# Performance work log

Measured on AMD Instinct MI355X. Metric: run time of the kernel, lower is better.

The kernel has to match this reference:

```python
import jax, jax.numpy as jnp
import numpy as np

B, C, W, H = 4, 256, 64, 64
CQK = C // 8  # 32


def setup_inputs() -> dict:
    key = jax.random.key(0)
    ks = jax.random.split(key, 8)
    scale = 0.02
    x = jax.random.normal(ks[0], (B, C, W, H), dtype=jnp.float32)
    wq = jax.random.normal(ks[1], (CQK, C), dtype=jnp.float32) * scale
    bq = jnp.zeros((CQK,), dtype=jnp.float32)
    wk = jax.random.normal(ks[2], (CQK, C), dtype=jnp.float32) * scale
    bk = jnp.zeros((CQK,), dtype=jnp.float32)
    wv = jax.random.normal(ks[3], (C, C), dtype=jnp.float32) * scale
    bv = jnp.zeros((C,), dtype=jnp.float32)
    gamma = jnp.zeros((1,), dtype=jnp.float32)
    return {"x": x, "wq": wq, "bq": bq, "wk": wk, "bk": bk,
            "wv": wv, "bv": bv, "gamma": gamma}


def reference(x, wq, bq, wk, bk, wv, bv, gamma):
    b, c, w, h = x.shape
    n = w * h
    xf = x.reshape(b, c, n)                         # b, C, N
    # 1x1 convs == channel matmuls
    q = jnp.einsum('oc,bcn->bno', wq, xf) + bq      # b, N, Cqk
    k = jnp.einsum('oc,bcn->bon', wk, xf) + bk[:, None]  # b, Cqk, N
    v = jnp.einsum('oc,bcn->bon', wv, xf) + bv[:, None]  # b, C, N
    energy = jnp.einsum('bic,bcj->bij', q, k)       # b, N, N
    attention = jax.nn.softmax(energy, axis=-1)     # b, N, N
    # out[b,c,i] = sum_j v[b,c,j] * attention[b,i,j]
    out = jnp.einsum('bcj,bij->bci', v, attention)  # b, C, N
    out = out.reshape(b, c, w, h)
    out = gamma[0] * out + x
    return out, attention
```

## Files before the change

### kernel.cpp

```cpp
#include <hip/hip_runtime.h>

#define NB 4
#define NC 256
#define NN 4096
#define NQK 32

typedef short short8 __attribute__((ext_vector_type(8)));
typedef float f32x4 __attribute__((ext_vector_type(4)));

#define MFMA16(a, b, c) __builtin_amdgcn_mfma_f32_16x16x32_bf16((a), (b), (c), 0, 0, 0)

__device__ __forceinline__ unsigned short f2bf(float f) {
  unsigned int u = __builtin_bit_cast(unsigned int, f);
  u += 0x7fffu + ((u >> 16) & 1u);
  return (unsigned short)(u >> 16);
}

__global__ void k_prep(const float* __restrict__ wq, const float* __restrict__ wk,
                       const float* __restrict__ wv,
                       unsigned short* __restrict__ wqb, unsigned short* __restrict__ wkb,
                       unsigned short* __restrict__ wvb) {
  int i = blockIdx.x * 256 + threadIdx.x;
  if (i < NQK * NC) { wqb[i] = f2bf(wq[i]); wkb[i] = f2bf(wk[i]); }
  wvb[i] = f2bf(wv[i]);
}

__global__ void k_tr(const float* __restrict__ x, unsigned short* __restrict__ xT) {
  __shared__ unsigned short lds[64][66];
  int b = blockIdx.z, c0 = blockIdx.y * 64, n0 = blockIdx.x * 64;
  int t = threadIdx.x;
  int nl = t & 63, cq = t >> 6;
  const float* xp = x + ((size_t)(b * NC + c0)) * NN + n0;
#pragma unroll
  for (int r = 0; r < 16; ++r) {
    int cl = r * 4 + cq;
    lds[cl][nl] = f2bf(xp[(size_t)cl * NN + nl]);
  }
  __syncthreads();
  unsigned short* xo = xT + ((size_t)(b * NN + n0)) * NC + c0;
#pragma unroll
  for (int r = 0; r < 16; ++r) {
    int n2 = r * 4 + cq;
    xo[(size_t)n2 * NC + nl] = lds[nl][n2];
  }
}

__global__ __launch_bounds__(256) void k_proj(
    const unsigned short* __restrict__ xT,
    const unsigned short* __restrict__ wqb, const unsigned short* __restrict__ wkb,
    const unsigned short* __restrict__ wvb,
    const float* __restrict__ bq, const float* __restrict__ bk,
    const float* __restrict__ bv,
    unsigned short* __restrict__ qb, unsigned short* __restrict__ kTb,
    unsigned short* __restrict__ vb) {
  __shared__ unsigned short ldsv[256][68];
  int b = blockIdx.y, n0 = blockIdx.x * 64;
  int t = threadIdx.x, w = t >> 6, l = t & 63, lm = l & 15, lk = l >> 4;
  f32x4 qa[2] = {}, ka[2] = {}, va[16] = {};
  const unsigned short* xrow = xT + ((size_t)(b * NN + n0 + w * 16 + lm)) * NC + lk * 8;
#pragma unroll
  for (int kk = 0; kk < 8; ++kk) {
    short8 a = *(const short8*)(xrow + kk * 32);
    const unsigned short* wqp = wqb + lm * NC + kk * 32 + lk * 8;
    const unsigned short* wkp = wkb + lm * NC + kk * 32 + lk * 8;
    qa[0] = MFMA16(a, *(const short8*)(wqp), qa[0]);
    qa[1] = MFMA16(a, *(const short8*)(wqp + 16 * NC), qa[1]);
    ka[0] = MFMA16(a, *(const short8*)(wkp), ka[0]);
    ka[1] = MFMA16(a, *(const short8*)(wkp + 16 * NC), ka[1]);
#pragma unroll
    for (int ct = 0; ct < 16; ++ct) {
      const unsigned short* wvp = wvb + (ct * 16 + lm) * NC + kk * 32 + lk * 8;
      va[ct] = MFMA16(a, *(const short8*)(wvp), va[ct]);
    }
  }
  int nrow = n0 + w * 16 + lk * 4;
#pragma unroll
  for (int f = 0; f < 2; ++f) {
    float bqv = bq[f * 16 + lm], bkv = bk[f * 16 + lm];
#pragma unroll
    for (int r = 0; r < 4; ++r) {
      size_t o = ((size_t)(b * NN + nrow + r)) * NQK + f * 16 + lm;
      qb[o] = f2bf(qa[f][r] + bqv);
      kTb[o] = f2bf(ka[f][r] + bkv);
    }
  }
#pragma unroll
  for (int ct = 0; ct < 16; ++ct) {
    float bvv = bv[ct * 16 + lm];
#pragma unroll
    for (int r = 0; r < 4; ++r)
      ldsv[ct * 16 + lm][w * 16 + lk * 4 + r] = f2bf(va[ct][r] + bvv);
  }
  __syncthreads();
#pragma unroll
  for (int rep = 0; rep < 64; ++rep) {
    int c = rep * 4 + (t >> 6);
    int n = t & 63;
    vb[((size_t)(b * NC + c)) * NN + n0 + n] = ldsv[c][n];
  }
}

__global__ __launch_bounds__(512) void k_attn(
    const unsigned short* __restrict__ qb, const unsigned short* __restrict__ kTb,
    const unsigned short* __restrict__ vb, const float* __restrict__ x,
    const float* __restrict__ gamma, float* __restrict__ out,
    float* __restrict__ attn) {
  __shared__ unsigned short ldsv[256][72];
  __shared__ unsigned short ldsp[64][72];
  __shared__ float ldsd[64][2];
  int b = blockIdx.y, i0 = blockIdx.x * 64;
  int t = threadIdx.x, w = t >> 6, l = t & 63, lm = l & 15, lk = l >> 4;
  int is = w & 3, jh = w >> 2;
  int cg = w & 3, ih = w >> 2;
  const f32x4 z = {0.f, 0.f, 0.f, 0.f};

  short8 qa = *(const short8*)(qb + ((size_t)(b * NN + i0 + is * 16 + lm)) * NQK + lk * 8);
  const unsigned short* kbase = kTb + (size_t)b * NN * NQK + lk * 8;

  float ds0[4] = {0.f, 0.f, 0.f, 0.f};
  for (int j0 = jh * 2048; j0 < jh * 2048 + 2048; j0 += 32) {
    short8 kf0 = *(const short8*)(kbase + (size_t)(j0 + lm) * NQK);
    short8 kf1 = *(const short8*)(kbase + (size_t)(j0 + 16 + lm) * NQK);
    f32x4 e0 = MFMA16(qa, kf0, z);
    f32x4 e1 = MFMA16(qa, kf1, z);
#pragma unroll
    for (int r = 0; r < 4; ++r) ds0[r] += __expf(e0[r]) + __expf(e1[r]);
  }
#pragma unroll
  for (int m = 1; m < 16; m <<= 1)
#pragma unroll
    for (int r = 0; r < 4; ++r) ds0[r] += __shfl_xor(ds0[r], m);
  if (lm == 0) {
#pragma unroll
    for (int r = 0; r < 4; ++r) ldsd[is * 16 + lk * 4 + r][jh] = ds0[r];
  }
  __syncthreads();
  float dinv[4];
#pragma unroll
  for (int r = 0; r < 4; ++r) {
    int row = is * 16 + lk * 4 + r;
    dinv[r] = 1.0f / (ldsd[row][0] + ldsd[row][1]);
  }

  f32x4 acc[4][2] = {};
  float g = gamma[0];
  float* attn_b = attn + (size_t)b * NN * NN;
  for (int j0 = 0; j0 < NN; j0 += 64) {
    __syncthreads();
#pragma unroll
    for (int it = 0; it < 4; ++it) {
      int qid = it * 512 + t;
      int row = qid >> 3, part = qid & 7;
      *(short8*)(&ldsv[row][part * 8]) =
          *(const short8*)(vb + ((size_t)(b * NC + row)) * NN + j0 + part * 8);
    }
    int jb = j0 + jh * 32;
    short8 kf0 = *(const short8*)(kbase + (size_t)(jb + lm) * NQK);
    short8 kf1 = *(const short8*)(kbase + (size_t)(jb + 16 + lm) * NQK);
    f32x4 e0 = MFMA16(qa, kf0, z);
    f32x4 e1 = MFMA16(qa, kf1, z);
    int irow = i0 + is * 16 + lk * 4;
#pragma unroll
    for (int r = 0; r < 4; ++r) {
      float p0 = __expf(e0[r]) * dinv[r];
      float p1 = __expf(e1[r]) * dinv[r];
      __builtin_nontemporal_store(p0, &attn_b[(size_t)(irow + r) * NN + jb + lm]);
      __builtin_nontemporal_store(p1, &attn_b[(size_t)(irow + r) * NN + jb + 16 + lm]);
      ldsp[is * 16 + lk * 4 + r][jh * 32 + lm] = f2bf(p0);
      ldsp[is * 16 + lk * 4 + r][jh * 32 + 16 + lm] = f2bf(p1);
    }
    __syncthreads();
#pragma unroll
    for (int kk = 0; kk < 2; ++kk) {
      short8 pf0 = *(const short8*)(&ldsp[ih * 32 + lm][kk * 32 + lk * 8]);
      short8 pf1 = *(const short8*)(&ldsp[ih * 32 + 16 + lm][kk * 32 + lk * 8]);
#pragma unroll
      for (int ct = 0; ct < 4; ++ct) {
        short8 af = *(const short8*)(&ldsv[cg * 64 + ct * 16 + lm][kk * 32 + lk * 8]);
        acc[ct][0] = MFMA16(af, pf0, acc[ct][0]);
        acc[ct][1] = MFMA16(af, pf1, acc[ct][1]);
      }
    }
  }
#pragma unroll
  for (int ct = 0; ct < 4; ++ct)
#pragma unroll
    for (int pt = 0; pt < 2; ++pt)
#pragma unroll
      for (int r = 0; r < 4; ++r) {
        int c = cg * 64 + ct * 16 + lk * 4 + r;
        int i = i0 + ih * 32 + pt * 16 + lm;
        size_t idx = ((size_t)(b * NC + c)) * NN + i;
        out[idx] = g * acc[ct][pt][r] + x[idx];
      }
}

extern "C" void kernel_launch(void* const* d_in, const int* in_sizes, int n_in,
                              void* d_out, int out_size, void* d_ws, size_t ws_size,
                              hipStream_t stream) {
  (void)in_sizes; (void)n_in; (void)out_size; (void)ws_size;
  const float* x  = (const float*)d_in[0];
  const float* wq = (const float*)d_in[1];
  const float* bq = (const float*)d_in[2];
  const float* wk = (const float*)d_in[3];
  const float* bk = (const float*)d_in[4];
  const float* wv = (const float*)d_in[5];
  const float* bv = (const float*)d_in[6];
  const float* gamma = (const float*)d_in[7];
  float* out  = (float*)d_out;
  float* attn = out + (size_t)NB * NC * NN;

  char* ws = (char*)d_ws;
  unsigned short* xT  = (unsigned short*)(ws);
  unsigned short* qb  = (unsigned short*)(ws + 8388608);
  unsigned short* kTb = (unsigned short*)(ws + 9437184);
  unsigned short* vb  = (unsigned short*)(ws + 10485760);
  unsigned short* wqb = (unsigned short*)(ws + 18874368);
  unsigned short* wkb = (unsigned short*)(ws + 18890752);
  unsigned short* wvb = (unsigned short*)(ws + 18907136);

  k_prep<<<dim3(256), dim3(256), 0, stream>>>(wq, wk, wv, wqb, wkb, wvb);
  k_tr<<<dim3(64, 4, 4), dim3(256), 0, stream>>>(x, xT);
  k_proj<<<dim3(64, 4), dim3(256), 0, stream>>>(xT, wqb, wkb, wvb, bq, bk, bv,
                                                qb, kTb, vb);
  k_attn<<<dim3(64, 4), dim3(512), 0, stream>>>(qb, kTb, vb, x, gamma, out, attn);
}
```

Before: 411.6 us.

## Fuse transpose into projection, double-buffer attention LDS, vectorize attention stores

Removes the separate x-transpose kernel: k_proj now loads fp32 x directly, converts it to bf16 and transposes it through LDS, splitting waves between the QK and V projections. The attention kernel double-buffers its V and P LDS tiles, which drops the leading barrier per iteration. It also remaps block indices and writes the attention matrix as coalesced 16-byte nontemporal stores read back from LDS. Softmax switches to exp2, with log2(e) folded into q. The stored attention values are now the bf16-rounded probabilities rather than the fp32 ones, which lowers output precision.

After: 396.0 us. 1.04x faster.

```diff
diff --git a/kernel.cpp b/kernel.cpp
--- a/kernel.cpp
+++ b/kernel.cpp
@@ -10,10 +10,22 @@
 
 #define MFMA16(a, b, c) __builtin_amdgcn_mfma_f32_16x16x32_bf16((a), (b), (c), 0, 0, 0)
 
+#if __has_builtin(__builtin_amdgcn_exp2f)
+#define EXP2(x) __builtin_amdgcn_exp2f(x)
+#else
+#define EXP2(x) __expf((x) * 0.6931471805599453f)
+#endif
+
+#define L2E 1.4426950408889634f
+
 __device__ __forceinline__ unsigned short f2bf(float f) {
   unsigned int u = __builtin_bit_cast(unsigned int, f);
   u += 0x7fffu + ((u >> 16) & 1u);
   return (unsigned short)(u >> 16);
+}
+__device__ __forceinline__ float bf2f(unsigned short u) {
+  unsigned int v = ((unsigned int)u) << 16;
+  return __builtin_bit_cast(float, v);
 }
 
 __global__ void k_prep(const float* __restrict__ wq, const float* __restrict__ wk,
@@ -25,78 +37,92 @@
   wvb[i] = f2bf(wv[i]);
 }
 
-__global__ void k_tr(const float* __restrict__ x, unsigned short* __restrict__ xT) {
-  __shared__ unsigned short lds[64][66];
-  int b = blockIdx.z, c0 = blockIdx.y * 64, n0 = blockIdx.x * 64;
-  int t = threadIdx.x;
-  int nl = t & 63, cq = t >> 6;
-  const float* xp = x + ((size_t)(b * NC + c0)) * NN + n0;
-#pragma unroll
-  for (int r = 0; r < 16; ++r) {
-    int cl = r * 4 + cq;
-    lds[cl][nl] = f2bf(xp[(size_t)cl * NN + nl]);
-  }
-  __syncthreads();
-  unsigned short* xo = xT + ((size_t)(b * NN + n0)) * NC + c0;
-#pragma unroll
-  for (int r = 0; r < 16; ++r) {
-    int n2 = r * 4 + cq;
-    xo[(size_t)n2 * NC + nl] = lds[nl][n2];
-  }
-}
-
 __global__ __launch_bounds__(256) void k_proj(
-    const unsigned short* __restrict__ xT,
+    const float* __restrict__ x,
     const unsigned short* __restrict__ wqb, const unsigned short* __restrict__ wkb,
     const unsigned short* __restrict__ wvb,
     const float* __restrict__ bq, const float* __restrict__ bk,
     const float* __restrict__ bv,
     unsigned short* __restrict__ qb, unsigned short* __restrict__ kTb,
     unsigned short* __restrict__ vb) {
-  __shared__ unsigned short ldsv[256][68];
-  int b = blockIdx.y, n0 = blockIdx.x * 64;
+  __shared__ unsigned short ldsx[32][264];
+  __shared__ unsigned short ldsvt[256][40];
+  int b = blockIdx.y, n0 = blockIdx.x * 32;
   int t = threadIdx.x, w = t >> 6, l = t & 63, lm = l & 15, lk = l >> 4;
-  f32x4 qa[2] = {}, ka[2] = {}, va[16] = {};
-  const unsigned short* xrow = xT + ((size_t)(b * NN + n0 + w * 16 + lm)) * NC + lk * 8;
-#pragma unroll
-  for (int kk = 0; kk < 8; ++kk) {
-    short8 a = *(const short8*)(xrow + kk * 32);
-    const unsigned short* wqp = wqb + lm * NC + kk * 32 + lk * 8;
-    const unsigned short* wkp = wkb + lm * NC + kk * 32 + lk * 8;
-    qa[0] = MFMA16(a, *(const short8*)(wqp), qa[0]);
-    qa[1] = MFMA16(a, *(const short8*)(wqp + 16 * NC), qa[1]);
-    ka[0] = MFMA16(a, *(const short8*)(wkp), ka[0]);
-    ka[1] = MFMA16(a, *(const short8*)(wkp + 16 * NC), ka[1]);
-#pragma unroll
-    for (int ct = 0; ct < 16; ++ct) {
-      const unsigned short* wvp = wvb + (ct * 16 + lm) * NC + kk * 32 + lk * 8;
-      va[ct] = MFMA16(a, *(const short8*)(wvp), va[ct]);
-    }
-  }
-  int nrow = n0 + w * 16 + lk * 4;
-#pragma unroll
-  for (int f = 0; f < 2; ++f) {
-    float bqv = bq[f * 16 + lm], bkv = bk[f * 16 + lm];
-#pragma unroll
-    for (int r = 0; r < 4; ++r) {
-      size_t o = ((size_t)(b * NN + nrow + r)) * NQK + f * 16 + lm;
-      qb[o] = f2bf(qa[f][r] + bqv);
-      kTb[o] = f2bf(ka[f][r] + bkv);
-    }
-  }
-#pragma unroll
-  for (int ct = 0; ct < 16; ++ct) {
-    float bvv = bv[ct * 16 + lm];
-#pragma unroll
-    for (int r = 0; r < 4; ++r)
-      ldsv[ct * 16 + lm][w * 16 + lk * 4 + r] = f2bf(va[ct][r] + bvv);
+  const float* xb = x + (size_t)b * NC * NN + n0;
+#pragma unroll
+  for (int p = 0; p < 8; ++p) {
+    int c = p * 32 + (t >> 3);
+    int n4 = (t & 7) * 4;
+    f32x4 v4 = *(const f32x4*)(xb + (size_t)c * NN + n4);
+#pragma unroll
+    for (int u = 0; u < 4; ++u) ldsx[n4 + u][c] = f2bf(v4[u]);
   }
   __syncthreads();
-#pragma unroll
-  for (int rep = 0; rep < 64; ++rep) {
-    int c = rep * 4 + (t >> 6);
-    int n = t & 63;
-    vb[((size_t)(b * NC + c)) * NN + n0 + n] = ldsv[c][n];
+  int s = w & 1, h = w >> 1;
+  f32x4 qa[2] = {}, ka[2] = {}, va[10] = {};
+  if (h == 0) {
+#pragma unroll
+    for (int kk = 0; kk < 8; ++kk) {
+      short8 a = *(const short8*)(&ldsx[s * 16 + lm][kk * 32 + lk * 8]);
+      const unsigned short* wqp = wqb + lm * NC + kk * 32 + lk * 8;
+      const unsigned short* wkp = wkb + lm * NC + kk * 32 + lk * 8;
+      qa[0] = MFMA16(a, *(const short8*)(wqp), qa[0]);
+      qa[1] = MFMA16(a, *(const short8*)(wqp + 16 * NC), qa[1]);
+      ka[0] = MFMA16(a, *(const short8*)(wkp), ka[0]);
+      ka[1] = MFMA16(a, *(const short8*)(wkp + 16 * NC), ka[1]);
+#pragma unroll
+      for (int j = 0; j < 6; ++j) {
+        const unsigned short* wvp = wvb + (size_t)(j * 16 + lm) * NC + kk * 32 + lk * 8;
+        va[j] = MFMA16(a, *(const short8*)(wvp), va[j]);
+      }
+    }
+  } else {
+#pragma unroll
+    for (int kk = 0; kk < 8; ++kk) {
+      short8 a = *(const short8*)(&ldsx[s * 16 + lm][kk * 32 + lk * 8]);
+#pragma unroll
+      for (int j = 0; j < 10; ++j) {
+        const unsigned short* wvp = wvb + (size_t)(96 + j * 16 + lm) * NC + kk * 32 + lk * 8;
+        va[j] = MFMA16(a, *(const short8*)(wvp), va[j]);
+      }
+    }
+  }
+  if (h == 0) {
+    int nrow = n0 + s * 16 + lk * 4;
+#pragma unroll
+    for (int f = 0; f < 2; ++f) {
+      float bqv = bq[f * 16 + lm], bkv = bk[f * 16 + lm];
+#pragma unroll
+      for (int r = 0; r < 4; ++r) {
+        size_t o = ((size_t)(b * NN + nrow + r)) * NQK + f * 16 + lm;
+        qb[o] = f2bf((qa[f][r] + bqv) * L2E);
+        kTb[o] = f2bf(ka[f][r] + bkv);
+      }
+    }
+#pragma unroll
+    for (int j = 0; j < 6; ++j) {
+      float bvv = bv[j * 16 + lm];
+#pragma unroll
+      for (int r = 0; r < 4; ++r)
+        ldsvt[j * 16 + lm][s * 16 + lk * 4 + r] = f2bf(va[j][r] + bvv);
+    }
+  } else {
+#pragma unroll
+    for (int j = 0; j < 10; ++j) {
+      float bvv = bv[96 + j * 16 + lm];
+#pragma unroll
+      for (int r = 0; r < 4; ++r)
+        ldsvt[96 + j * 16 + lm][s * 16 + lk * 4 + r] = f2bf(va[j][r] + bvv);
+    }
+  }
+  __syncthreads();
+#pragma unroll
+  for (int p = 0; p < 4; ++p) {
+    int c = p * 64 + (t >> 2);
+    int np = (t & 3) * 8;
+    *(short8*)(vb + ((size_t)(b * NC + c)) * NN + n0 + np) =
+        *(const short8*)(&ldsvt[c][np]);
   }
 }
 
@@ -105,10 +131,12 @@
     const unsigned short* __restrict__ vb, const float* __restrict__ x,
     const float* __restrict__ gamma, float* __restrict__ out,
     float* __restrict__ attn) {
-  __shared__ unsigned short ldsv[256][72];
-  __shared__ unsigned short ldsp[64][72];
+  __shared__ unsigned short ldsv[2][256][72];
+  __shared__ unsigned short ldsp[2][64][72];
   __shared__ float ldsd[64][2];
-  int b = blockIdx.y, i0 = blockIdx.x * 64;
+  int id = blockIdx.x;
+  int b = (id >> 1) & 3;
+  int i0 = (((id >> 3) << 1) | (id & 1)) * 64;
   int t = threadIdx.x, w = t >> 6, l = t & 63, lm = l & 15, lk = l >> 4;
   int is = w & 3, jh = w >> 2;
   int cg = w & 3, ih = w >> 2;
@@ -118,13 +146,14 @@
   const unsigned short* kbase = kTb + (size_t)b * NN * NQK + lk * 8;
 
   float ds0[4] = {0.f, 0.f, 0.f, 0.f};
+#pragma unroll 4
   for (int j0 = jh * 2048; j0 < jh * 2048 + 2048; j0 += 32) {
     short8 kf0 = *(const short8*)(kbase + (size_t)(j0 + lm) * NQK);
     short8 kf1 = *(const short8*)(kbase + (size_t)(j0 + 16 + lm) * NQK);
     f32x4 e0 = MFMA16(qa, kf0, z);
     f32x4 e1 = MFMA16(qa, kf1, z);
 #pragma unroll
-    for (int r = 0; r < 4; ++r) ds0[r] += __expf(e0[r]) + __expf(e1[r]);
+    for (int r = 0; r < 4; ++r) ds0[r] += EXP2(e0[r]) + EXP2(e1[r]);
   }
 #pragma unroll
   for (int m = 1; m < 16; m <<= 1)
@@ -145,38 +174,47 @@
   f32x4 acc[4][2] = {};
   float g = gamma[0];
   float* attn_b = attn + (size_t)b * NN * NN;
-  for (int j0 = 0; j0 < NN; j0 += 64) {
-    __syncthreads();
+  const unsigned short* vbb = vb + (size_t)b * NC * NN;
+  for (int tt = 0; tt < 64; ++tt) {
+    int p = tt & 1;
+    int j0 = tt * 64;
 #pragma unroll
     for (int it = 0; it < 4; ++it) {
       int qid = it * 512 + t;
       int row = qid >> 3, part = qid & 7;
-      *(short8*)(&ldsv[row][part * 8]) =
-          *(const short8*)(vb + ((size_t)(b * NC + row)) * NN + j0 + part * 8);
+      *(short8*)(&ldsv[p][row][part * 8]) =
+          *(const short8*)(vbb + (size_t)row * NN + j0 + part * 8);
     }
     int jb = j0 + jh * 32;
     short8 kf0 = *(const short8*)(kbase + (size_t)(jb + lm) * NQK);
     short8 kf1 = *(const short8*)(kbase + (size_t)(jb + 16 + lm) * NQK);
     f32x4 e0 = MFMA16(qa, kf0, z);
     f32x4 e1 = MFMA16(qa, kf1, z);
-    int irow = i0 + is * 16 + lk * 4;
 #pragma unroll
     for (int r = 0; r < 4; ++r) {
-      float p0 = __expf(e0[r]) * dinv[r];
-      float p1 = __expf(e1[r]) * dinv[r];
-      __builtin_nontemporal_store(p0, &attn_b[(size_t)(irow + r) * NN + jb + lm]);
-      __builtin_nontemporal_store(p1, &attn_b[(size_t)(irow + r) * NN + jb + 16 + lm]);
-      ldsp[is * 16 + lk * 4 + r][jh * 32 + lm] = f2bf(p0);
-      ldsp[is * 16 + lk * 4 + r][jh * 32 + 16 + lm] = f2bf(p1);
+      float p0 = EXP2(e0[r]) * dinv[r];
+      float p1 = EXP2(e1[r]) * dinv[r];
+      int il = is * 16 + lk * 4 + r;
+      ldsp[p][il][jh * 32 + lm] = f2bf(p0);
+      ldsp[p][il][jh * 32 + 16 + lm] = f2bf(p1);
     }
     __syncthreads();
 #pragma unroll
+    for (int q2 = 0; q2 < 2; ++q2) {
+      int row = q2 * 32 + (t >> 4);
+      int jl = (t & 15) * 4;
+      f32x4 vo;
+#pragma unroll
+      for (int u = 0; u < 4; ++u) vo[u] = bf2f(ldsp[p][row][jl + u]);
+      __builtin_nontemporal_store(vo, (f32x4*)(attn_b + (size_t)(i0 + row) * NN + j0 + jl));
+    }
+#pragma unroll
     for (int kk = 0; kk < 2; ++kk) {
-      short8 pf0 = *(const short8*)(&ldsp[ih * 32 + lm][kk * 32 + lk * 8]);
-      short8 pf1 = *(const short8*)(&ldsp[ih * 32 + 16 + lm][kk * 32 + lk * 8]);
+      short8 pf0 = *(const short8*)(&ldsp[p][ih * 32 + lm][kk * 32 + lk * 8]);
+      short8 pf1 = *(const short8*)(&ldsp[p][ih * 32 + 16 + lm][kk * 32 + lk * 8]);
 #pragma unroll
       for (int ct = 0; ct < 4; ++ct) {
-        short8 af = *(const short8*)(&ldsv[cg * 64 + ct * 16 + lm][kk * 32 + lk * 8]);
+        short8 af = *(const short8*)(&ldsv[p][cg * 64 + ct * 16 + lm][kk * 32 + lk * 8]);
         acc[ct][0] = MFMA16(af, pf0, acc[ct][0]);
         acc[ct][1] = MFMA16(af, pf1, acc[ct][1]);
       }
@@ -211,17 +249,15 @@
   float* attn = out + (size_t)NB * NC * NN;
 
   char* ws = (char*)d_ws;
-  unsigned short* xT  = (unsigned short*)(ws);
-  unsigned short* qb  = (unsigned short*)(ws + 8388608);
-  unsigned short* kTb = (unsigned short*)(ws + 9437184);
-  unsigned short* vb  = (unsigned short*)(ws + 10485760);
-  unsigned short* wqb = (unsigned short*)(ws + 18874368);
-  unsigned short* wkb = (unsigned short*)(ws + 18890752);
-  unsigned short* wvb = (unsigned short*)(ws + 18907136);
+  unsigned short* qb  = (unsigned short*)(ws);
+  unsigned short* kTb = (unsigned short*)(ws + 1048576);
+  unsigned short* vb  = (unsigned short*)(ws + 2097152);
+  unsigned short* wqb = (unsigned short*)(ws + 10485760);
+  unsigned short* wkb = (unsigned short*)(ws + 10502144);
+  unsigned short* wvb = (unsigned short*)(ws + 10518528);
 
   k_prep<<<dim3(256), dim3(256), 0, stream>>>(wq, wk, wv, wqb, wkb, wvb);
-  k_tr<<<dim3(64, 4, 4), dim3(256), 0, stream>>>(x, xT);
-  k_proj<<<dim3(64, 4), dim3(256), 0, stream>>>(xT, wqb, wkb, wvb, bq, bk, bv,
-                                                qb, kTb, vb);
-  k_attn<<<dim3(64, 4), dim3(512), 0, stream>>>(qb, kTb, vb, x, gamma, out, attn);
-}
+  k_proj<<<dim3(128, 4), dim3(256), 0, stream>>>(x, wqb, wkb, wvb, bq, bk, bv,
+                                                 qb, kTb, vb);
+  k_attn<<<dim3(256), dim3(512), 0, stream>>>(qb, kTb, vb, x, gamma, out, attn);
+}
```
